# Kernel optimization log

Measured on AMD Instinct MI355X. Metric: run time of the kernel, lower is better.

## Reference

```python
import jax, jax.numpy as jnp
import numpy as np

N_NODES = 50000
N_REL = 4
N_EDGES = 400000
IN_F, HID_F, OUT_F = 128, 128, 64


def _graphconv(h, s, d, W, b, n_nodes):
    """DGL GraphConv, norm='both': D_dst^{-1/2} A D_src^{-1/2} h W + b.
    Degrees clamped to min 1 (DGL behavior for isolated nodes)."""
    ones = jnp.ones(s.shape[0], h.dtype)
    deg_out = jnp.clip(jax.ops.segment_sum(ones, s, num_segments=n_nodes), 1.0)
    deg_in = jnp.clip(jax.ops.segment_sum(ones, d, num_segments=n_nodes), 1.0)
    # scale src features, transform first (weight applied pre-aggregation)
    hw = (h * jax.lax.rsqrt(deg_out)[:, None]) @ W          # [N, out]
    msg = hw[s]                                              # gather  [E, out]
    agg = jax.ops.segment_sum(msg, d, num_segments=n_nodes)  # scatter [N, out]
    return agg * jax.lax.rsqrt(deg_in)[:, None] + b


def _hetero_layer(h, src, dst, W, b):
    # HeteroGraphConv with aggregate='sum': sum per-relation GraphConv outputs
    n_nodes = h.shape[0]
    out = _graphconv(h, src[0], dst[0], W[0], b[0], n_nodes)
    for r in range(1, W.shape[0]):
        out = out + _graphconv(h, src[r], dst[r], W[r], b[r], n_nodes)
    return out


def setup_inputs() -> dict:
    key = jax.random.key(0)
    k = jax.random.split(key, 6)
    x = jax.random.normal(k[0], (N_NODES, IN_F), dtype=jnp.float32)
    src = jax.random.randint(k[1], (N_REL, N_EDGES), 0, N_NODES, dtype=jnp.int32)
    dst = jax.random.randint(k[2], (N_REL, N_EDGES), 0, N_NODES, dtype=jnp.int32)
    W1 = jax.random.normal(k[3], (N_REL, IN_F, HID_F), dtype=jnp.float32) / np.sqrt(IN_F)
    b1 = jnp.zeros((N_REL, HID_F), dtype=jnp.float32)
    W2 = jax.random.normal(k[4], (N_REL, HID_F, OUT_F), dtype=jnp.float32) / np.sqrt(HID_F)
    b2 = jnp.zeros((N_REL, OUT_F), dtype=jnp.float32)
    return {"x": x, "src": src, "dst": dst, "W1": W1, "b1": b1, "W2": W2, "b2": b2}


def reference(x, src, dst, W1, b1, W2, b2):
    h = _hetero_layer(x, src, dst, W1, b1)
    h = jax.nn.relu(h)
    return _hetero_layer(h, src, dst, W2, b2)
```

## Files before the change

### kernel.cpp

```cpp
#include <hip/hip_runtime.h>
#include <hip/hip_bf16.h>

#define N_NODES 50000
#define N_REL 4
#define N_EDGES 400000
#define CHUNK 1024
#define NCHUNK ((N_NODES + CHUNK - 1) / CHUNK)

#define EB 32
#define ECH (N_EDGES / EB)
#define NR 8
#define RNG (N_NODES / NR)

using short8 = __attribute__((ext_vector_type(8))) short;
using f32x4 = __attribute__((ext_vector_type(4))) float;

static __device__ inline unsigned short f2bf(float f) {
  unsigned u = __float_as_uint(f);
  unsigned r = (u + 0x7FFFu + ((u >> 16) & 1u)) >> 16;
  return (unsigned short)r;
}
static __device__ inline float bf2f(unsigned short b) {
  return __uint_as_float(((unsigned)b) << 16);
}
static __device__ inline void fma_bf2(unsigned w, float ds, float& a0,
                                      float& a1) {
  float lo = __uint_as_float(w << 16);
  float hi = __uint_as_float(w & 0xffff0000u);
  a0 = fmaf(lo, ds, a0);
  a1 = fmaf(hi, ds, a1);
}

__global__ __launch_bounds__(256) void k_hist(const int* __restrict__ src,
                                              const int* __restrict__ dst,
                                              unsigned short* __restrict__ Hs,
                                              unsigned short* __restrict__ Hd) {
  const int range = blockIdx.x % NR;
  const int chunk = (blockIdx.x / NR) % EB;
  const int rel = blockIdx.x / (NR * EB);
  __shared__ unsigned int ldsS[RNG / 2], ldsD[RNG / 2];
  for (int i = threadIdx.x; i < RNG / 2; i += 256) {
    ldsS[i] = 0u;
    ldsD[i] = 0u;
  }
  __syncthreads();
  const int n0 = range * RNG;
  const int* sp = src + (size_t)rel * N_EDGES + chunk * ECH;
  const int* dp = dst + (size_t)rel * N_EDGES + chunk * ECH;
  for (int e = threadIdx.x; e < ECH; e += 256) {
    int s = sp[e] - n0;
    if ((unsigned)s < RNG) atomicAdd(&ldsS[s >> 1], 1u << ((s & 1) * 16));
    int d = dp[e] - n0;
    if ((unsigned)d < RNG) atomicAdd(&ldsD[d >> 1], 1u << ((d & 1) * 16));
  }
  __syncthreads();
  unsigned int* HsO =
      (unsigned int*)(Hs + ((size_t)rel * EB + chunk) * N_NODES + n0);
  unsigned int* HdO =
      (unsigned int*)(Hd + ((size_t)rel * EB + chunk) * N_NODES + n0);
  for (int i = threadIdx.x; i < RNG / 2; i += 256) {
    HsO[i] = ldsS[i];
    HdO[i] = ldsD[i];
  }
}

__global__ __launch_bounds__(256) void k_reduce_m(
    const unsigned short* __restrict__ Hs, unsigned short* __restrict__ Hd,
    int* __restrict__ cnt_m, float* __restrict__ dso, float* __restrict__ dsi,
    ushort4* __restrict__ relOff) {
  int n = blockIdx.x * 256 + threadIdx.x;
  if (n >= N_NODES) return;
#pragma unroll
  for (int r = 0; r < N_REL; ++r) {
    int so = 0;
#pragma unroll
    for (int b = 0; b < EB; ++b) so += Hs[((size_t)r * EB + b) * N_NODES + n];
    dso[r * N_NODES + n] = rsqrtf((float)(so < 1 ? 1 : so));
  }
  int run = 0;
  unsigned short rs[4];
#pragma unroll
  for (int r = 0; r < N_REL; ++r) {
    rs[r] = (unsigned short)run;
#pragma unroll
    for (int b = 0; b < EB; ++b) {
      size_t off = ((size_t)r * EB + b) * N_NODES + n;
      int v = Hd[off];
      Hd[off] = (unsigned short)run;
      run += v;
    }
    int di = run - rs[r];
    dsi[r * N_NODES + n] = rsqrtf((float)(di < 1 ? 1 : di));
  }
  cnt_m[n] = run;
  relOff[n] = make_ushort4(rs[0], rs[1], rs[2], rs[3]);
}

__global__ __launch_bounds__(256) void k_chunk_sums(
    const int* __restrict__ cnt_m, int* __restrict__ chunkSums) {
  int c = blockIdx.x;
  int t = threadIdx.x;
  int base = c * CHUNK + t * 4;
  int s = 0;
#pragma unroll
  for (int j = 0; j < 4; ++j) {
    int n = base + j;
    if (n < N_NODES) s += cnt_m[n];
  }
  __shared__ int lds[256];
  lds[t] = s;
  __syncthreads();
  for (int off = 128; off > 0; off >>= 1) {
    if (t < off) lds[t] += lds[t + off];
    __syncthreads();
  }
  if (t == 0) chunkSums[c] = lds[0];
}

__global__ __launch_bounds__(64) void k_scan_chunks(int* __restrict__ chunkSums,
                                                    int* __restrict__ row_ptr) {
  if (threadIdx.x == 0) {
    int running = 0;
    for (int c = 0; c < NCHUNK; ++c) {
      int v = chunkSums[c];
      chunkSums[c] = running;
      running += v;
    }
    row_ptr[N_NODES] = N_REL * N_EDGES;
  }
}

__global__ __launch_bounds__(256) void k_scan_within(
    const int* __restrict__ cnt_m, const int* __restrict__ chunkOff,
    int* __restrict__ row_ptr) {
  int c = blockIdx.x;
  int t = threadIdx.x;
  int base = c * CHUNK + t * 4;
  int v[4];
#pragma unroll
  for (int j = 0; j < 4; ++j) {
    int n = base + j;
    v[j] = (n < N_NODES) ? cnt_m[n] : 0;
  }
  int total = v[0] + v[1] + v[2] + v[3];
  __shared__ int lds[256];
  lds[t] = total;
  __syncthreads();
  for (int off = 1; off < 256; off <<= 1) {
    int add = (t >= off) ? lds[t - off] : 0;
    __syncthreads();
    lds[t] += add;
    __syncthreads();
  }
  int thrExcl = lds[t] - total + chunkOff[c];
  int pre = 0;
#pragma unroll
  for (int j = 0; j < 4; ++j) {
    int n = base + j;
    if (n < N_NODES) row_ptr[n] = thrExcl + pre;
    pre += v[j];
  }
}

__global__ __launch_bounds__(256) void k_fill2m(
    const int* __restrict__ src, const int* __restrict__ dst,
    const unsigned short* __restrict__ Hd, const int* __restrict__ row_ptr,
    int* __restrict__ sorted) {
  const int range = blockIdx.x % NR;
  const int chunk = (blockIdx.x / NR) % EB;
  const int rel = blockIdx.x / (NR * EB);
  __shared__ unsigned int cur[RNG];
  const int n0 = range * RNG;
  const int* rp = row_ptr + n0;
  const unsigned short* pref = Hd + ((size_t)rel * EB + chunk) * N_NODES + n0;
  for (int i = threadIdx.x; i < RNG; i += 256)
    cur[i] = (unsigned)(rp[i] + pref[i]);
  __syncthreads();
  const int* sp = src + (size_t)rel * N_EDGES + chunk * ECH;
  const int* dp = dst + (size_t)rel * N_EDGES + chunk * ECH;
  for (int e = threadIdx.x; e < ECH; e += 256) {
    int d = dp[e] - n0;
    if ((unsigned)d < RNG) {
      unsigned pos = atomicAdd(&cur[d], 1u);
      sorted[pos] = sp[e];
    }
  }
}

__global__ __launch_bounds__(256) void k_prep_x(const float* __restrict__ x,
                                                unsigned short* __restrict__ xb) {
  int i = blockIdx.x * 256 + threadIdx.x;
  if (i >= N_NODES * 16) return;
  const float4* p = (const float4*)x + (size_t)i * 2;
  float4 v0 = p[0], v1 = p[1];
  unsigned short pk[8] = {f2bf(v0.x), f2bf(v0.y), f2bf(v0.z), f2bf(v0.w),
                          f2bf(v1.x), f2bf(v1.y), f2bf(v1.z), f2bf(v1.w)};
  *(uint4*)(xb + (size_t)i * 8) = *(uint4*)pk;
}

__global__ __launch_bounds__(128) void k_prep_w(const float* __restrict__ W1,
                                                const float* __restrict__ W2,
                                                unsigned short* __restrict__ Wt1,
                                                unsigned short* __restrict__ Wt2) {
  int b = blockIdx.x;
  int kk = threadIdx.x;
  if (b < 128) {
    int c = b;
#pragma unroll
    for (int r = 0; r < 4; ++r)
      Wt1[(size_t)c * 512 + r * 128 + kk] =
          f2bf(W1[(size_t)r * 16384 + kk * 128 + c]);
  } else {
    int c = b - 128;
    int r = c >> 6, cc = c & 63;
    Wt2[(size_t)c * 128 + kk] = f2bf(W2[(size_t)r * 8192 + kk * 64 + cc]);
  }
}

__global__ __launch_bounds__(256) void k_gather1a(
    const unsigned short* __restrict__ xb, const int* __restrict__ row_ptr,
    const ushort4* __restrict__ relOff, const int* __restrict__ sortedm,
    const float* __restrict__ dso, const float* __restrict__ dsi,
    unsigned int* __restrict__ agg) {
  const int wave = threadIdx.x >> 6, lane = threadIdx.x & 63;
  const int g = lane & 31;
  const int node = blockIdx.x * 8 + wave * 2 + (lane >> 5);
  const int rp = row_ptr[node], rp1 = row_ptr[node + 1];
  const ushort4 ro = relOff[node];
  const int beg[4] = {rp + ro.x, rp + ro.y, rp + ro.z, rp + ro.w};
  const int end4[4] = {rp + ro.y, rp + ro.z, rp + ro.w, rp1};
#pragma unroll
  for (int r = 0; r < 4; ++r) {
    const float* dsoR = dso + (size_t)r * N_NODES;
    float a0[4] = {0, 0, 0, 0}, a1[4] = {0, 0, 0, 0};
    float a2[4] = {0, 0, 0, 0}, a3[4] = {0, 0, 0, 0};
    for (int base = beg[r]; base < end4[r]; base += 32) {
      int n = end4[r] - base;
      if (n > 32) n = 32;
      int my = (g < n) ? sortedm[base + g] : 0;
      int j = 0;
      for (; j + 3 < n; j += 4) {
#pragma unroll
        for (int k = 0; k < 4; ++k) {
          int s = __shfl(my, j + k, 32);
          float ds = dsoR[s];
          uint2 w = *(const uint2*)(xb + (size_t)s * 128 + g * 4);
          fma_bf2(w.x, ds, a0[k], a1[k]);
          fma_bf2(w.y, ds, a2[k], a3[k]);
        }
      }
      for (; j < n; ++j) {
        int s = __shfl(my, j, 32);
        float ds = dsoR[s];
        uint2 w = *(const uint2*)(xb + (size_t)s * 128 + g * 4);
        fma_bf2(w.x, ds, a0[0], a1[0]);
        fma_bf2(w.y, ds, a2[0], a3[0]);
      }
    }
    float di = dsi[(size_t)r * N_NODES + node];
    float t0 = ((a0[0] + a0[1]) + (a0[2] + a0[3])) * di;
    float t1 = ((a1[0] + a1[1]) + (a1[2] + a1[3])) * di;
    float t2 = ((a2[0] + a2[1]) + (a2[2] + a2[3])) * di;
    float t3 = ((a3[0] + a3[1]) + (a3[2] + a3[3])) * di;
    uint2 pk;
    pk.x = (unsigned)f2bf(t0) | ((unsigned)f2bf(t1) << 16);
    pk.y = (unsigned)f2bf(t2) | ((unsigned)f2bf(t3) << 16);
    *((uint2*)agg + ((size_t)node * 4 + r) * 32 + g) = pk;
  }
}

__global__ __launch_bounds__(256, 2) void k_gemm_h1(
    const unsigned short* __restrict__ agg, const unsigned short* __restrict__ Wt,
    const float* __restrict__ b1, unsigned short* __restrict__ h1, int M) {
  __shared__ unsigned short Alds[64 * 128];
  __shared__ unsigned short Wlds[128 * 128];
  const int tid = threadIdx.x;
  const int wid = tid >> 6, lane = tid & 63;
  const int rowBase = blockIdx.x * 64;
  const int lrow = lane & 15;
  const int quarter = lane >> 4;

  f32x4 acc[4][2];
#pragma unroll
  for (int i = 0; i < 4; ++i)
#pragma unroll
    for (int j = 0; j < 2; ++j) acc[i][j] = (f32x4){0.f, 0.f, 0.f, 0.f};

  for (int k0 = 0; k0 < 4; ++k0) {
    __syncthreads();
#pragma unroll
    for (int it = 0; it < 4; ++it) {
      int cid = tid + it * 256;
      int row = cid >> 4, kg = cid & 15;
      int grow = rowBase + row;
      uint4 v = make_uint4(0, 0, 0, 0);
      if (grow < M)
        v = *(const uint4*)(agg + (size_t)grow * 512 + k0 * 128 + kg * 8);
      *(uint4*)(Alds + row * 128 + ((kg ^ (row & 7)) * 8)) = v;
    }
#pragma unroll
    for (int it = 0; it < 8; ++it) {
      int cid = tid + it * 256;
      int c = cid >> 4, kg = cid & 15;
      uint4 v = *(const uint4*)(Wt + (size_t)c * 512 + k0 * 128 + kg * 8);
      *(uint4*)(Wlds + c * 128 + ((kg ^ (c & 7)) * 8)) = v;
    }
    __syncthreads();
#pragma unroll
    for (int kk = 0; kk < 4; ++kk) {
      int kg = kk * 4 + quarter;
      short8 a[4], b[2];
#pragma unroll
      for (int i = 0; i < 4; ++i) {
        int row = i * 16 + lrow;
        a[i] = *(const short8*)(Alds + row * 128 + ((kg ^ (row & 7)) * 8));
      }
#pragma unroll
      for (int j = 0; j < 2; ++j) {
        int c = wid * 32 + j * 16 + lrow;
        b[j] = *(const short8*)(Wlds + c * 128 + ((kg ^ (c & 7)) * 8));
      }
#pragma unroll
      for (int i = 0; i < 4; ++i)
#pragma unroll
        for (int j = 0; j < 2; ++j)
          acc[i][j] = __builtin_amdgcn_mfma_f32_16x16x32_bf16(a[i], b[j],
                                                              acc[i][j], 0, 0, 0);
    }
  }

#pragma unroll
  for (int j = 0; j < 2; ++j) {
    int c = wid * 32 + j * 16 + lrow;
    float bs = b1[c] + b1[128 + c] + b1[256 + c] + b1[384 + c];
#pragma unroll
    for (int i = 0; i < 4; ++i) {
#pragma unroll
      for (int r = 0; r < 4; ++r) {
        int grow = rowBase + i * 16 + quarter * 4 + r;
        if (grow < M)
          h1[(size_t)grow * 128 + c] = f2bf(fmaxf(acc[i][j][r] + bs, 0.f));
      }
    }
  }
}

template <int REL_COLS>
__global__ __launch_bounds__(256, 2) void k_gemm_mfma(
    const unsigned short* __restrict__ A, const unsigned short* __restrict__ Wt,
    const float* __restrict__ dsoBase, unsigned short* __restrict__ C,
    int cstride, int M) {
  __shared__ unsigned short Alds[64 * 128];
  __shared__ unsigned short Wlds[256 * 128];
  const int tid = threadIdx.x;
  const int wid = tid >> 6, lane = tid & 63;
  const int rowBase = blockIdx.x * 64;

#pragma unroll
  for (int i = 0; i < 4; ++i) {
    int cid = tid + i * 256;
    int row = cid >> 4, kg = cid & 15;
    int grow = rowBase + row;
    uint4 v = make_uint4(0, 0, 0, 0);
    if (grow < M) v = *(const uint4*)(A + (size_t)grow * 128 + kg * 8);
    *(uint4*)(Alds + row * 128 + ((kg ^ (row & 7)) * 8)) = v;
  }
#pragma unroll
  for (int i = 0; i < 16; ++i) {
    int cid = tid + i * 256;
    int row = cid >> 4, kg = cid & 15;
    uint4 v = *(const uint4*)(Wt + (size_t)row * 128 + kg * 8);
    *(uint4*)(Wlds + row * 128 + ((kg ^ (row & 7)) * 8)) = v;
  }
  __syncthreads();

  f32x4 acc[4][4];
#pragma unroll
  for (int i = 0; i < 4; ++i)
#pragma unroll
    for (int j = 0; j < 4; ++j) acc[i][j] = (f32x4){0.f, 0.f, 0.f, 0.f};

  const int lrow = lane & 15;
  const int khalf = lane >> 4;
#pragma unroll
  for (int k0 = 0; k0 < 4; ++k0) {
    int kg = k0 * 4 + khalf;
    short8 a[4], b[4];
#pragma unroll
    for (int i = 0; i < 4; ++i) {
      int row = i * 16 + lrow;
      a[i] = *(const short8*)(Alds + row * 128 + ((kg ^ (row & 7)) * 8));
    }
#pragma unroll
    for (int j = 0; j < 4; ++j) {
      int wrow = wid * 64 + j * 16 + lrow;
      b[j] = *(const short8*)(Wlds + wrow * 128 + ((kg ^ (wrow & 7)) * 8));
    }
#pragma unroll
    for (int i = 0; i < 4; ++i)
#pragma unroll
      for (int j = 0; j < 4; ++j)
        acc[i][j] = __builtin_amdgcn_mfma_f32_16x16x32_bf16(a[i], b[j],
                                                            acc[i][j], 0, 0, 0);
  }

#pragma unroll
  for (int i = 0; i < 4; ++i) {
#pragma unroll
    for (int j = 0; j < 4; ++j) {
      int col = wid * 64 + j * 16 + (lane & 15);
      const float* dsoCol = dsoBase + (size_t)(col / REL_COLS) * N_NODES;
#pragma unroll
      for (int r = 0; r < 4; ++r) {
        int grow = rowBase + i * 16 + (lane >> 4) * 4 + r;
        if (grow < M)
          C[(size_t)grow * cstride + col] = f2bf(acc[i][j][r] * dsoCol[grow]);
      }
    }
  }
}

__global__ __launch_bounds__(256) void k_gather2m(
    const unsigned short* __restrict__ Y, const int* __restrict__ row_ptr,
    const ushort4* __restrict__ relOff, const int* __restrict__ sortedm,
    const float* __restrict__ dsi, const float* __restrict__ b2,
    float* __restrict__ out) {
  const int wave = threadIdx.x >> 6, lane = threadIdx.x & 63;
  const int g = lane & 15;
  const int node = blockIdx.x * 16 + wave * 4 + (lane >> 4);
  const int rp = row_ptr[node], rp1 = row_ptr[node + 1];
  const ushort4 ro = relOff[node];
  const int beg[4] = {rp + ro.x, rp + ro.y, rp + ro.z, rp + ro.w};
  const int end4[4] = {rp + ro.y, rp + ro.z, rp + ro.w, rp1};
  float t0 = 0.f, t1 = 0.f, t2 = 0.f, t3 = 0.f;
#pragma unroll
  for (int r = 0; r < 4; ++r) {
    float a0[4] = {0, 0, 0, 0}, a1[4] = {0, 0, 0, 0};
    float a2[4] = {0, 0, 0, 0}, a3[4] = {0, 0, 0, 0};
    for (int base = beg[r]; base < end4[r]; base += 16) {
      int n = end4[r] - base;
      if (n > 16) n = 16;
      int my = (g < n) ? sortedm[base + g] : 0;
      int j = 0;
      for (; j + 3 < n; j += 4) {
#pragma unroll
        for (int k = 0; k < 4; ++k) {
          int s = __shfl(my, j + k, 16);
          uint2 w = *(const uint2*)(Y + ((size_t)s * 4 + r) * 64 + g * 4);
          fma_bf2(w.x, 1.f, a0[k], a1[k]);
          fma_bf2(w.y, 1.f, a2[k], a3[k]);
        }
      }
      for (; j < n; ++j) {
        int s = __shfl(my, j, 16);
        uint2 w = *(const uint2*)(Y + ((size_t)s * 4 + r) * 64 + g * 4);
        fma_bf2(w.x, 1.f, a0[0], a1[0]);
        fma_bf2(w.y, 1.f, a2[0], a3[0]);
      }
    }
    float di = dsi[(size_t)r * N_NODES + node];
    t0 = fmaf((a0[0] + a0[1]) + (a0[2] + a0[3]), di, t0);
    t1 = fmaf((a1[0] + a1[1]) + (a1[2] + a1[3]), di, t1);
    t2 = fmaf((a2[0] + a2[1]) + (a2[2] + a2[3]), di, t2);
    t3 = fmaf((a3[0] + a3[1]) + (a3[2] + a3[3]), di, t3);
  }
#pragma unroll
  for (int r = 0; r < 4; ++r) {
    float4 bb = *(const float4*)(b2 + r * 64 + g * 4);
    t0 += bb.x;
    t1 += bb.y;
    t2 += bb.z;
    t3 += bb.w;
  }
  *(float4*)(out + (size_t)node * 64 + g * 4) = make_float4(t0, t1, t2, t3);
}

extern "C" void kernel_launch(void* const* d_in, const int* in_sizes, int n_in,
                              void* d_out, int out_size, void* d_ws,
                              size_t ws_size, hipStream_t stream) {
  const float* x  = (const float*)d_in[0];
  const int* src  = (const int*)d_in[1];
  const int* dst  = (const int*)d_in[2];
  const float* W1 = (const float*)d_in[3];
  const float* b1 = (const float*)d_in[4];
  const float* W2 = (const float*)d_in[5];
  const float* b2 = (const float*)d_in[6];
  float* out = (float*)d_out;

  char* wsb = (char*)d_ws;
  unsigned short* Hs = (unsigned short*)wsb;
  unsigned short* h1 = (unsigned short*)wsb;
  unsigned short* Hd = Hs + (size_t)N_REL * EB * N_NODES;
  unsigned short* xb = Hd + (size_t)N_REL * EB * N_NODES;
  unsigned short* agg = xb + (size_t)N_NODES * 128;
  unsigned short* Y2 = agg;
  char* tail = (char*)(agg + (size_t)N_NODES * 512);
  unsigned short* Wt1 = (unsigned short*)tail;
  unsigned short* Wt2 = Wt1 + 128 * 512;
  float* dso = (float*)(Wt2 + 256 * 128);
  float* dsi = dso + N_REL * N_NODES;
  ushort4* relOff = (ushort4*)(dsi + N_REL * N_NODES);
  int* cnt_m = (int*)(relOff + N_NODES);
  int* row_ptr = cnt_m + N_NODES;
  int* chunkSums = row_ptr + (N_NODES + 1);
  int* sorted = chunkSums + 64;

  k_prep_x<<<(N_NODES * 16 + 255) / 256, 256, 0, stream>>>(x, xb);
  k_prep_w<<<384, 128, 0, stream>>>(W1, W2, Wt1, Wt2);
  k_hist<<<N_REL * EB * NR, 256, 0, stream>>>(src, dst, Hs, Hd);
  k_reduce_m<<<(N_NODES + 255) / 256, 256, 0, stream>>>(Hs, Hd, cnt_m, dso,
                                                        dsi, relOff);
  k_chunk_sums<<<NCHUNK, 256, 0, stream>>>(cnt_m, chunkSums);
  k_scan_chunks<<<1, 64, 0, stream>>>(chunkSums, row_ptr);
  k_scan_within<<<NCHUNK, 256, 0, stream>>>(cnt_m, chunkSums, row_ptr);
  k_fill2m<<<N_REL * EB * NR, 256, 0, stream>>>(src, dst, Hd, row_ptr, sorted);

  k_gather1a<<<N_NODES / 8, 256, 0, stream>>>(xb, row_ptr, relOff, sorted, dso,
                                              dsi, (unsigned int*)agg);
  k_gemm_h1<<<(N_NODES + 63) / 64, 256, 0, stream>>>(agg, Wt1, b1, h1,
                                                     N_NODES);
  k_gemm_mfma<64><<<(N_NODES + 63) / 64, 256, 0, stream>>>(h1, Wt2, dso, Y2,
                                                           256, N_NODES);
  k_gather2m<<<N_NODES / 16, 256, 0, stream>>>(Y2, row_ptr, relOff, sorted,
                                               dsi, b2, out);
}
```

Baseline: 275.2 us.

## Fuse prep and histogram kernels, fold chunk sums into reduce, flatten gather loops

Merges the x conversion, weight transpose and degree histogram kernels into one launch, and folds the per-chunk edge-count sum into the degree-reduce kernel through block reductions plus atomics. This removes two kernel launches and their serialization gaps. Both gather kernels now walk a node's whole edge list in a single windowed loop that switches relation at boundaries. This replaces separate per-relation loops that each reloaded index windows and underfilled the shuffle windows. The price is heavier per-block divergence in the fused kernel and extra branching inside the gather loops.

```diff
diff --git a/kernel.cpp b/kernel.cpp
--- a/kernel.cpp
+++ b/kernel.cpp
@@ -11,6 +11,10 @@
 #define ECH (N_EDGES / EB)
 #define NR 8
 #define RNG (N_NODES / NR)
+
+#define PX_BLOCKS 3125
+#define PW_BLOCKS 192
+#define HIST_BLOCKS (N_REL * EB * NR)
 
 using short8 = __attribute__((ext_vector_type(8))) short;
 using f32x4 = __attribute__((ext_vector_type(4))) float;
@@ -31,15 +35,47 @@
   a1 = fmaf(hi, ds, a1);
 }
 
-__global__ __launch_bounds__(256) void k_hist(const int* __restrict__ src,
-                                              const int* __restrict__ dst,
-                                              unsigned short* __restrict__ Hs,
-                                              unsigned short* __restrict__ Hd) {
-  const int range = blockIdx.x % NR;
-  const int chunk = (blockIdx.x / NR) % EB;
-  const int rel = blockIdx.x / (NR * EB);
+__global__ __launch_bounds__(256) void k_prep_fused(
+    const float* __restrict__ x, const float* __restrict__ W1,
+    const float* __restrict__ W2, const int* __restrict__ src,
+    const int* __restrict__ dst, unsigned short* __restrict__ xb,
+    unsigned short* __restrict__ Wt1, unsigned short* __restrict__ Wt2,
+    unsigned short* __restrict__ Hs, unsigned short* __restrict__ Hd,
+    int* __restrict__ chunkSums) {
   __shared__ unsigned int ldsS[RNG / 2], ldsD[RNG / 2];
-  for (int i = threadIdx.x; i < RNG / 2; i += 256) {
+  const int b = blockIdx.x;
+  const int tid = threadIdx.x;
+  if (b < PX_BLOCKS) {
+    if (b == 0 && tid < 64) chunkSums[tid] = 0;
+    int i = b * 256 + tid;
+    const float4* p = (const float4*)x + (size_t)i * 2;
+    float4 v0 = p[0], v1 = p[1];
+    unsigned short pk[8] = {f2bf(v0.x), f2bf(v0.y), f2bf(v0.z), f2bf(v0.w),
+                            f2bf(v1.x), f2bf(v1.y), f2bf(v1.z), f2bf(v1.w)};
+    *(uint4*)(xb + (size_t)i * 8) = *(uint4*)pk;
+    return;
+  }
+  if (b < PX_BLOCKS + PW_BLOCKS) {
+    int ob = (b - PX_BLOCKS) * 2 + (tid >> 7);
+    int kk = tid & 127;
+    if (ob < 128) {
+      int c = ob;
+#pragma unroll
+      for (int r = 0; r < 4; ++r)
+        Wt1[(size_t)c * 512 + r * 128 + kk] =
+            f2bf(W1[(size_t)r * 16384 + kk * 128 + c]);
+    } else {
+      int c = ob - 128;
+      int r = c >> 6, cc = c & 63;
+      Wt2[(size_t)c * 128 + kk] = f2bf(W2[(size_t)r * 8192 + kk * 64 + cc]);
+    }
+    return;
+  }
+  const int hb = b - PX_BLOCKS - PW_BLOCKS;
+  const int range = hb % NR;
+  const int chunk = (hb / NR) % EB;
+  const int rel = hb / (NR * EB);
+  for (int i = tid; i < RNG / 2; i += 256) {
     ldsS[i] = 0u;
     ldsD[i] = 0u;
   }
@@ -47,7 +83,7 @@
   const int n0 = range * RNG;
   const int* sp = src + (size_t)rel * N_EDGES + chunk * ECH;
   const int* dp = dst + (size_t)rel * N_EDGES + chunk * ECH;
-  for (int e = threadIdx.x; e < ECH; e += 256) {
+  for (int e = tid; e < ECH; e += 256) {
     int s = sp[e] - n0;
     if ((unsigned)s < RNG) atomicAdd(&ldsS[s >> 1], 1u << ((s & 1) * 16));
     int d = dp[e] - n0;
@@ -58,7 +94,7 @@
       (unsigned int*)(Hs + ((size_t)rel * EB + chunk) * N_NODES + n0);
   unsigned int* HdO =
       (unsigned int*)(Hd + ((size_t)rel * EB + chunk) * N_NODES + n0);
-  for (int i = threadIdx.x; i < RNG / 2; i += 256) {
+  for (int i = tid; i < RNG / 2; i += 256) {
     HsO[i] = ldsS[i];
     HdO[i] = ldsD[i];
   }
@@ -67,54 +103,43 @@
 __global__ __launch_bounds__(256) void k_reduce_m(
     const unsigned short* __restrict__ Hs, unsigned short* __restrict__ Hd,
     int* __restrict__ cnt_m, float* __restrict__ dso, float* __restrict__ dsi,
-    ushort4* __restrict__ relOff) {
+    ushort4* __restrict__ relOff, int* __restrict__ chunkSums) {
   int n = blockIdx.x * 256 + threadIdx.x;
-  if (n >= N_NODES) return;
-#pragma unroll
-  for (int r = 0; r < N_REL; ++r) {
-    int so = 0;
-#pragma unroll
-    for (int b = 0; b < EB; ++b) so += Hs[((size_t)r * EB + b) * N_NODES + n];
-    dso[r * N_NODES + n] = rsqrtf((float)(so < 1 ? 1 : so));
-  }
   int run = 0;
-  unsigned short rs[4];
-#pragma unroll
-  for (int r = 0; r < N_REL; ++r) {
-    rs[r] = (unsigned short)run;
-#pragma unroll
-    for (int b = 0; b < EB; ++b) {
-      size_t off = ((size_t)r * EB + b) * N_NODES + n;
-      int v = Hd[off];
-      Hd[off] = (unsigned short)run;
-      run += v;
-    }
-    int di = run - rs[r];
-    dsi[r * N_NODES + n] = rsqrtf((float)(di < 1 ? 1 : di));
-  }
-  cnt_m[n] = run;
-  relOff[n] = make_ushort4(rs[0], rs[1], rs[2], rs[3]);
-}
-
-__global__ __launch_bounds__(256) void k_chunk_sums(
-    const int* __restrict__ cnt_m, int* __restrict__ chunkSums) {
-  int c = blockIdx.x;
-  int t = threadIdx.x;
-  int base = c * CHUNK + t * 4;
-  int s = 0;
-#pragma unroll
-  for (int j = 0; j < 4; ++j) {
-    int n = base + j;
-    if (n < N_NODES) s += cnt_m[n];
-  }
-  __shared__ int lds[256];
-  lds[t] = s;
+  if (n < N_NODES) {
+#pragma unroll
+    for (int r = 0; r < N_REL; ++r) {
+      int so = 0;
+#pragma unroll
+      for (int b = 0; b < EB; ++b)
+        so += Hs[((size_t)r * EB + b) * N_NODES + n];
+      dso[r * N_NODES + n] = rsqrtf((float)(so < 1 ? 1 : so));
+    }
+    unsigned short rs[4];
+#pragma unroll
+    for (int r = 0; r < N_REL; ++r) {
+      rs[r] = (unsigned short)run;
+#pragma unroll
+      for (int b = 0; b < EB; ++b) {
+        size_t off = ((size_t)r * EB + b) * N_NODES + n;
+        int v = Hd[off];
+        Hd[off] = (unsigned short)run;
+        run += v;
+      }
+      int di = run - rs[r];
+      dsi[r * N_NODES + n] = rsqrtf((float)(di < 1 ? 1 : di));
+    }
+    cnt_m[n] = run;
+    relOff[n] = make_ushort4(rs[0], rs[1], rs[2], rs[3]);
+  }
+  __shared__ int red[256];
+  red[threadIdx.x] = run;
   __syncthreads();
   for (int off = 128; off > 0; off >>= 1) {
-    if (t < off) lds[t] += lds[t + off];
+    if (threadIdx.x < off) red[threadIdx.x] += red[threadIdx.x + off];
     __syncthreads();
   }
-  if (t == 0) chunkSums[c] = lds[0];
+  if (threadIdx.x == 0) atomicAdd(&chunkSums[blockIdx.x >> 2], red[0]);
 }
 
 __global__ __launch_bounds__(64) void k_scan_chunks(int* __restrict__ chunkSums,
@@ -187,36 +212,6 @@
   }
 }
 
-__global__ __launch_bounds__(256) void k_prep_x(const float* __restrict__ x,
-                                                unsigned short* __restrict__ xb) {
-  int i = blockIdx.x * 256 + threadIdx.x;
-  if (i >= N_NODES * 16) return;
-  const float4* p = (const float4*)x + (size_t)i * 2;
-  float4 v0 = p[0], v1 = p[1];
-  unsigned short pk[8] = {f2bf(v0.x), f2bf(v0.y), f2bf(v0.z), f2bf(v0.w),
-                          f2bf(v1.x), f2bf(v1.y), f2bf(v1.z), f2bf(v1.w)};
-  *(uint4*)(xb + (size_t)i * 8) = *(uint4*)pk;
-}
-
-__global__ __launch_bounds__(128) void k_prep_w(const float* __restrict__ W1,
-                                                const float* __restrict__ W2,
-                                                unsigned short* __restrict__ Wt1,
-                                                unsigned short* __restrict__ Wt2) {
-  int b = blockIdx.x;
-  int kk = threadIdx.x;
-  if (b < 128) {
-    int c = b;
-#pragma unroll
-    for (int r = 0; r < 4; ++r)
-      Wt1[(size_t)c * 512 + r * 128 + kk] =
-          f2bf(W1[(size_t)r * 16384 + kk * 128 + c]);
-  } else {
-    int c = b - 128;
-    int r = c >> 6, cc = c & 63;
-    Wt2[(size_t)c * 128 + kk] = f2bf(W2[(size_t)r * 8192 + kk * 64 + cc]);
-  }
-}
-
 __global__ __launch_bounds__(256) void k_gather1a(
     const unsigned short* __restrict__ xb, const int* __restrict__ row_ptr,
     const ushort4* __restrict__ relOff, const int* __restrict__ sortedm,
@@ -225,47 +220,90 @@
   const int wave = threadIdx.x >> 6, lane = threadIdx.x & 63;
   const int g = lane & 31;
   const int node = blockIdx.x * 8 + wave * 2 + (lane >> 5);
-  const int rp = row_ptr[node], rp1 = row_ptr[node + 1];
-  const ushort4 ro = relOff[node];
-  const int beg[4] = {rp + ro.x, rp + ro.y, rp + ro.z, rp + ro.w};
-  const int end4[4] = {rp + ro.y, rp + ro.z, rp + ro.w, rp1};
-#pragma unroll
-  for (int r = 0; r < 4; ++r) {
-    const float* dsoR = dso + (size_t)r * N_NODES;
-    float a0[4] = {0, 0, 0, 0}, a1[4] = {0, 0, 0, 0};
-    float a2[4] = {0, 0, 0, 0}, a3[4] = {0, 0, 0, 0};
-    for (int base = beg[r]; base < end4[r]; base += 32) {
-      int n = end4[r] - base;
-      if (n > 32) n = 32;
-      int my = (g < n) ? sortedm[base + g] : 0;
-      int j = 0;
-      for (; j + 3 < n; j += 4) {
+  const int rp = row_ptr[node];
+  const int nt = row_ptr[node + 1] - rp;
+  const ushort4 ro4 = relOff[node];
+  const int rb1 = ro4.y, rb2 = ro4.z, rb3 = ro4.w;
+
+  float rs[4][4];
+#pragma unroll
+  for (int r = 0; r < 4; ++r)
+#pragma unroll
+    for (int f = 0; f < 4; ++f) rs[r][f] = 0.f;
+  float acc[4][4];
+#pragma unroll
+  for (int f = 0; f < 4; ++f)
+#pragma unroll
+    for (int k = 0; k < 4; ++k) acc[f][k] = 0.f;
+
+#define FLUSH1(RR)                                                     \
+  {                                                                    \
+    rs[RR][0] += (acc[0][0] + acc[0][1]) + (acc[0][2] + acc[0][3]);    \
+    rs[RR][1] += (acc[1][0] + acc[1][1]) + (acc[1][2] + acc[1][3]);    \
+    rs[RR][2] += (acc[2][0] + acc[2][1]) + (acc[2][2] + acc[2][3]);    \
+    rs[RR][3] += (acc[3][0] + acc[3][1]) + (acc[3][2] + acc[3][3]);    \
+    _Pragma("unroll") for (int f = 0; f < 4; ++f)                      \
+        _Pragma("unroll") for (int k = 0; k < 4; ++k) acc[f][k] = 0.f; \
+  }
+
+  int r = 0;
+  int rend = rb1;
+  for (int w0 = 0; w0 < nt; w0 += 32) {
+    int wn = nt - w0;
+    if (wn > 32) wn = 32;
+    int my = (g < wn) ? sortedm[rp + w0 + g] : 0;
+    int j = 0;
+    while (j < wn) {
+      while (w0 + j >= rend) {
+        switch (r) {
+          case 0: FLUSH1(0); break;
+          case 1: FLUSH1(1); break;
+          default: FLUSH1(2); break;
+        }
+        ++r;
+        rend = (r == 1) ? rb2 : (r == 2) ? rb3 : nt;
+      }
+      int lim = rend - w0;
+      if (lim > wn) lim = wn;
+      const float* dsoR = dso + (size_t)r * N_NODES;
+      for (; j + 3 < lim; j += 4) {
 #pragma unroll
         for (int k = 0; k < 4; ++k) {
           int s = __shfl(my, j + k, 32);
           float ds = dsoR[s];
           uint2 w = *(const uint2*)(xb + (size_t)s * 128 + g * 4);
-          fma_bf2(w.x, ds, a0[k], a1[k]);
-          fma_bf2(w.y, ds, a2[k], a3[k]);
+          fma_bf2(w.x, ds, acc[0][k], acc[1][k]);
+          fma_bf2(w.y, ds, acc[2][k], acc[3][k]);
         }
       }
-      for (; j < n; ++j) {
+      for (; j < lim; ++j) {
         int s = __shfl(my, j, 32);
         float ds = dsoR[s];
         uint2 w = *(const uint2*)(xb + (size_t)s * 128 + g * 4);
-        fma_bf2(w.x, ds, a0[0], a1[0]);
-        fma_bf2(w.y, ds, a2[0], a3[0]);
-      }
-    }
-    float di = dsi[(size_t)r * N_NODES + node];
-    float t0 = ((a0[0] + a0[1]) + (a0[2] + a0[3])) * di;
-    float t1 = ((a1[0] + a1[1]) + (a1[2] + a1[3])) * di;
-    float t2 = ((a2[0] + a2[1]) + (a2[2] + a2[3])) * di;
-    float t3 = ((a3[0] + a3[1]) + (a3[2] + a3[3])) * di;
+        fma_bf2(w.x, ds, acc[0][0], acc[1][0]);
+        fma_bf2(w.y, ds, acc[2][0], acc[3][0]);
+      }
+    }
+  }
+  switch (r) {
+    case 0: FLUSH1(0); break;
+    case 1: FLUSH1(1); break;
+    case 2: FLUSH1(2); break;
+    default: FLUSH1(3); break;
+  }
+#undef FLUSH1
+
+  float dia[4] = {dsi[node], dsi[N_NODES + node], dsi[2 * N_NODES + node],
+                  dsi[3 * N_NODES + node]};
+#pragma unroll
+  for (int rr = 0; rr < 4; ++rr) {
+    float di = dia[rr];
     uint2 pk;
-    pk.x = (unsigned)f2bf(t0) | ((unsigned)f2bf(t1) << 16);
-    pk.y = (unsigned)f2bf(t2) | ((unsigned)f2bf(t3) << 16);
-    *((uint2*)agg + ((size_t)node * 4 + r) * 32 + g) = pk;
+    pk.x = (unsigned)f2bf(rs[rr][0] * di) |
+           ((unsigned)f2bf(rs[rr][1] * di) << 16);
+    pk.y = (unsigned)f2bf(rs[rr][2] * di) |
+           ((unsigned)f2bf(rs[rr][3] * di) << 16);
+    *((uint2*)agg + ((size_t)node * 4 + rr) * 32 + g) = pk;
   }
 }
 
@@ -428,51 +466,85 @@
   const int wave = threadIdx.x >> 6, lane = threadIdx.x & 63;
   const int g = lane & 15;
   const int node = blockIdx.x * 16 + wave * 4 + (lane >> 4);
-  const int rp = row_ptr[node], rp1 = row_ptr[node + 1];
-  const ushort4 ro = relOff[node];
-  const int beg[4] = {rp + ro.x, rp + ro.y, rp + ro.z, rp + ro.w};
-  const int end4[4] = {rp + ro.y, rp + ro.z, rp + ro.w, rp1};
-  float t0 = 0.f, t1 = 0.f, t2 = 0.f, t3 = 0.f;
-#pragma unroll
-  for (int r = 0; r < 4; ++r) {
-    float a0[4] = {0, 0, 0, 0}, a1[4] = {0, 0, 0, 0};
-    float a2[4] = {0, 0, 0, 0}, a3[4] = {0, 0, 0, 0};
-    for (int base = beg[r]; base < end4[r]; base += 16) {
-      int n = end4[r] - base;
-      if (n > 16) n = 16;
-      int my = (g < n) ? sortedm[base + g] : 0;
-      int j = 0;
-      for (; j + 3 < n; j += 4) {
+  const int rp = row_ptr[node];
+  const int nt = row_ptr[node + 1] - rp;
+  const ushort4 ro4 = relOff[node];
+  const int rb1 = ro4.y, rb2 = ro4.z, rb3 = ro4.w;
+  const float dia[4] = {dsi[node], dsi[N_NODES + node],
+                        dsi[2 * N_NODES + node], dsi[3 * N_NODES + node]};
+
+  float t[4] = {0.f, 0.f, 0.f, 0.f};
+  float acc[4][4];
+#pragma unroll
+  for (int f = 0; f < 4; ++f)
+#pragma unroll
+    for (int k = 0; k < 4; ++k) acc[f][k] = 0.f;
+
+#define FLUSH2(RR)                                                          \
+  {                                                                         \
+    float di = dia[RR];                                                     \
+    t[0] = fmaf((acc[0][0] + acc[0][1]) + (acc[0][2] + acc[0][3]), di, t[0]); \
+    t[1] = fmaf((acc[1][0] + acc[1][1]) + (acc[1][2] + acc[1][3]), di, t[1]); \
+    t[2] = fmaf((acc[2][0] + acc[2][1]) + (acc[2][2] + acc[2][3]), di, t[2]); \
+    t[3] = fmaf((acc[3][0] + acc[3][1]) + (acc[3][2] + acc[3][3]), di, t[3]); \
+    _Pragma("unroll") for (int f = 0; f < 4; ++f)                           \
+        _Pragma("unroll") for (int k = 0; k < 4; ++k) acc[f][k] = 0.f;      \
+  }
+
+  int r = 0;
+  int rend = rb1;
+  for (int w0 = 0; w0 < nt; w0 += 16) {
+    int wn = nt - w0;
+    if (wn > 16) wn = 16;
+    int my = (g < wn) ? sortedm[rp + w0 + g] : 0;
+    int j = 0;
+    while (j < wn) {
+      while (w0 + j >= rend) {
+        switch (r) {
+          case 0: FLUSH2(0); break;
+          case 1: FLUSH2(1); break;
+          default: FLUSH2(2); break;
+        }
+        ++r;
+        rend = (r == 1) ? rb2 : (r == 2) ? rb3 : nt;
+      }
+      int lim = rend - w0;
+      if (lim > wn) lim = wn;
+      for (; j + 3 < lim; j += 4) {
 #pragma unroll
         for (int k = 0; k < 4; ++k) {
           int s = __shfl(my, j + k, 16);
           uint2 w = *(const uint2*)(Y + ((size_t)s * 4 + r) * 64 + g * 4);
-          fma_bf2(w.x, 1.f, a0[k], a1[k]);
-          fma_bf2(w.y, 1.f, a2[k], a3[k]);
+          fma_bf2(w.x, 1.f, acc[0][k], acc[1][k]);
+          fma_bf2(w.y, 1.f, acc[2][k], acc[3][k]);
         }
       }
-      for (; j < n; ++j) {
+      for (; j < lim; ++j) {
         int s = __shfl(my, j, 16);
         uint2 w = *(const uint2*)(Y + ((size_t)s * 4 + r) * 64 + g * 4);
-        fma_bf2(w.x, 1.f, a0[0], a1[0]);
-        fma_bf2(w.y, 1.f, a2[0], a3[0]);
-      }
-    }
-    float di = dsi[(size_t)r * N_NODES + node];
-    t0 = fmaf((a0[0] + a0[1]) + (a0[2] + a0[3]), di, t0);
-    t1 = fmaf((a1[0] + a1[1]) + (a1[2] + a1[3]), di, t1);
-    t2 = fmaf((a2[0] + a2[1]) + (a2[2] + a2[3]), di, t2);
-    t3 = fmaf((a3[0] + a3[1]) + (a3[2] + a3[3]), di, t3);
-  }
-#pragma unroll
-  for (int r = 0; r < 4; ++r) {
-    float4 bb = *(const float4*)(b2 + r * 64 + g * 4);
-    t0 += bb.x;
-    t1 += bb.y;
-    t2 += bb.z;
-    t3 += bb.w;
-  }
-  *(float4*)(out + (size_t)node * 64 + g * 4) = make_float4(t0, t1, t2, t3);
+        fma_bf2(w.x, 1.f, acc[0][0], acc[1][0]);
+        fma_bf2(w.y, 1.f, acc[2][0], acc[3][0]);
+      }
+    }
+  }
+  switch (r) {
+    case 0: FLUSH2(0); break;
+    case 1: FLUSH2(1); break;
+    case 2: FLUSH2(2); break;
+    default: FLUSH2(3); break;
+  }
+#undef FLUSH2
+
+#pragma unroll
+  for (int rr = 0; rr < 4; ++rr) {
+    float4 bb = *(const float4*)(b2 + rr * 64 + g * 4);
+    t[0] += bb.x;
+    t[1] += bb.y;
+    t[2] += bb.z;
+    t[3] += bb.w;
+  }
+  *(float4*)(out + (size_t)node * 64 + g * 4) =
+      make_float4(t[0], t[1], t[2], t[3]);
 }
 
 extern "C" void kernel_launch(void* const* d_in, const int* in_sizes, int n_in,
@@ -505,12 +577,10 @@
   int* chunkSums = row_ptr + (N_NODES + 1);
   int* sorted = chunkSums + 64;
 
-  k_prep_x<<<(N_NODES * 16 + 255) / 256, 256, 0, stream>>>(x, xb);
-  k_prep_w<<<384, 128, 0, stream>>>(W1, W2, Wt1, Wt2);
-  k_hist<<<N_REL * EB * NR, 256, 0, stream>>>(src, dst, Hs, Hd);
+  k_prep_fused<<<PX_BLOCKS + PW_BLOCKS + HIST_BLOCKS, 256, 0, stream>>>(
+      x, W1, W2, src, dst, xb, Wt1, Wt2, Hs, Hd, chunkSums);
   k_reduce_m<<<(N_NODES + 255) / 256, 256, 0, stream>>>(Hs, Hd, cnt_m, dso,
-                                                        dsi, relOff);
-  k_chunk_sums<<<NCHUNK, 256, 0, stream>>>(cnt_m, chunkSums);
+                                                        dsi, relOff, chunkSums);
   k_scan_chunks<<<1, 64, 0, stream>>>(chunkSums, row_ptr);
   k_scan_within<<<NCHUNK, 256, 0, stream>>>(cnt_m, chunkSums, row_ptr);
   k_fill2m<<<N_REL * EB * NR, 256, 0, stream>>>(src, dst, Hd, row_ptr, sorted);
```

Result: faster. 267.2 us (-2.9%).

## Fuse prep kernels, fold chunk sums into reduce, split gather1 by feature quarter

Applied to the files above, without the earlier changes.

Merges the x/W bf16 conversion and the degree histogram into one kernel, and folds the per-chunk sum into k_reduce_m using atomics. Together these remove two launches. The layer-1 gather is restructured so that 8 lanes per node each handle a 32-feature quarter, with four block groups covering the quarters. This raises node-level parallelism and shrinks the per-batch edge window, but it rereads the edge lists and degree scales once per quarter.

```diff
diff --git a/kernel.cpp b/kernel.cpp
--- a/kernel.cpp
+++ b/kernel.cpp
@@ -11,6 +11,12 @@
 #define ECH (N_EDGES / EB)
 #define NR 8
 #define RNG (N_NODES / NR)
+
+#define PX_BLOCKS 3125
+#define PW_BLOCKS 192
+#define HIST_BLOCKS (N_REL * EB * NR)
+
+#define G1_BLOCKS 1563
 
 using short8 = __attribute__((ext_vector_type(8))) short;
 using f32x4 = __attribute__((ext_vector_type(4))) float;
@@ -31,15 +37,47 @@
   a1 = fmaf(hi, ds, a1);
 }
 
-__global__ __launch_bounds__(256) void k_hist(const int* __restrict__ src,
-                                              const int* __restrict__ dst,
-                                              unsigned short* __restrict__ Hs,
-                                              unsigned short* __restrict__ Hd) {
-  const int range = blockIdx.x % NR;
-  const int chunk = (blockIdx.x / NR) % EB;
-  const int rel = blockIdx.x / (NR * EB);
+__global__ __launch_bounds__(256) void k_prep_fused(
+    const float* __restrict__ x, const float* __restrict__ W1,
+    const float* __restrict__ W2, const int* __restrict__ src,
+    const int* __restrict__ dst, unsigned short* __restrict__ xb,
+    unsigned short* __restrict__ Wt1, unsigned short* __restrict__ Wt2,
+    unsigned short* __restrict__ Hs, unsigned short* __restrict__ Hd,
+    int* __restrict__ chunkSums) {
   __shared__ unsigned int ldsS[RNG / 2], ldsD[RNG / 2];
-  for (int i = threadIdx.x; i < RNG / 2; i += 256) {
+  const int b = blockIdx.x;
+  const int tid = threadIdx.x;
+  if (b < PX_BLOCKS) {
+    if (b == 0 && tid < 64) chunkSums[tid] = 0;
+    int i = b * 256 + tid;
+    const float4* p = (const float4*)x + (size_t)i * 2;
+    float4 v0 = p[0], v1 = p[1];
+    unsigned short pk[8] = {f2bf(v0.x), f2bf(v0.y), f2bf(v0.z), f2bf(v0.w),
+                            f2bf(v1.x), f2bf(v1.y), f2bf(v1.z), f2bf(v1.w)};
+    *(uint4*)(xb + (size_t)i * 8) = *(uint4*)pk;
+    return;
+  }
+  if (b < PX_BLOCKS + PW_BLOCKS) {
+    int ob = (b - PX_BLOCKS) * 2 + (tid >> 7);
+    int kk = tid & 127;
+    if (ob < 128) {
+      int c = ob;
+#pragma unroll
+      for (int r = 0; r < 4; ++r)
+        Wt1[(size_t)c * 512 + r * 128 + kk] =
+            f2bf(W1[(size_t)r * 16384 + kk * 128 + c]);
+    } else {
+      int c = ob - 128;
+      int r = c >> 6, cc = c & 63;
+      Wt2[(size_t)c * 128 + kk] = f2bf(W2[(size_t)r * 8192 + kk * 64 + cc]);
+    }
+    return;
+  }
+  const int hb = b - PX_BLOCKS - PW_BLOCKS;
+  const int range = hb % NR;
+  const int chunk = (hb / NR) % EB;
+  const int rel = hb / (NR * EB);
+  for (int i = tid; i < RNG / 2; i += 256) {
     ldsS[i] = 0u;
     ldsD[i] = 0u;
   }
@@ -47,7 +85,7 @@
   const int n0 = range * RNG;
   const int* sp = src + (size_t)rel * N_EDGES + chunk * ECH;
   const int* dp = dst + (size_t)rel * N_EDGES + chunk * ECH;
-  for (int e = threadIdx.x; e < ECH; e += 256) {
+  for (int e = tid; e < ECH; e += 256) {
     int s = sp[e] - n0;
     if ((unsigned)s < RNG) atomicAdd(&ldsS[s >> 1], 1u << ((s & 1) * 16));
     int d = dp[e] - n0;
@@ -58,7 +96,7 @@
       (unsigned int*)(Hs + ((size_t)rel * EB + chunk) * N_NODES + n0);
   unsigned int* HdO =
       (unsigned int*)(Hd + ((size_t)rel * EB + chunk) * N_NODES + n0);
-  for (int i = threadIdx.x; i < RNG / 2; i += 256) {
+  for (int i = tid; i < RNG / 2; i += 256) {
     HsO[i] = ldsS[i];
     HdO[i] = ldsD[i];
   }
@@ -67,54 +105,43 @@
 __global__ __launch_bounds__(256) void k_reduce_m(
     const unsigned short* __restrict__ Hs, unsigned short* __restrict__ Hd,
     int* __restrict__ cnt_m, float* __restrict__ dso, float* __restrict__ dsi,
-    ushort4* __restrict__ relOff) {
+    ushort4* __restrict__ relOff, int* __restrict__ chunkSums) {
   int n = blockIdx.x * 256 + threadIdx.x;
-  if (n >= N_NODES) return;
-#pragma unroll
-  for (int r = 0; r < N_REL; ++r) {
-    int so = 0;
-#pragma unroll
-    for (int b = 0; b < EB; ++b) so += Hs[((size_t)r * EB + b) * N_NODES + n];
-    dso[r * N_NODES + n] = rsqrtf((float)(so < 1 ? 1 : so));
-  }
   int run = 0;
-  unsigned short rs[4];
-#pragma unroll
-  for (int r = 0; r < N_REL; ++r) {
-    rs[r] = (unsigned short)run;
-#pragma unroll
-    for (int b = 0; b < EB; ++b) {
-      size_t off = ((size_t)r * EB + b) * N_NODES + n;
-      int v = Hd[off];
-      Hd[off] = (unsigned short)run;
-      run += v;
-    }
-    int di = run - rs[r];
-    dsi[r * N_NODES + n] = rsqrtf((float)(di < 1 ? 1 : di));
-  }
-  cnt_m[n] = run;
-  relOff[n] = make_ushort4(rs[0], rs[1], rs[2], rs[3]);
-}
-
-__global__ __launch_bounds__(256) void k_chunk_sums(
-    const int* __restrict__ cnt_m, int* __restrict__ chunkSums) {
-  int c = blockIdx.x;
-  int t = threadIdx.x;
-  int base = c * CHUNK + t * 4;
-  int s = 0;
-#pragma unroll
-  for (int j = 0; j < 4; ++j) {
-    int n = base + j;
-    if (n < N_NODES) s += cnt_m[n];
-  }
-  __shared__ int lds[256];
-  lds[t] = s;
+  if (n < N_NODES) {
+#pragma unroll
+    for (int r = 0; r < N_REL; ++r) {
+      int so = 0;
+#pragma unroll
+      for (int b = 0; b < EB; ++b)
+        so += Hs[((size_t)r * EB + b) * N_NODES + n];
+      dso[r * N_NODES + n] = rsqrtf((float)(so < 1 ? 1 : so));
+    }
+    unsigned short rs[4];
+#pragma unroll
+    for (int r = 0; r < N_REL; ++r) {
+      rs[r] = (unsigned short)run;
+#pragma unroll
+      for (int b = 0; b < EB; ++b) {
+        size_t off = ((size_t)r * EB + b) * N_NODES + n;
+        int v = Hd[off];
+        Hd[off] = (unsigned short)run;
+        run += v;
+      }
+      int di = run - rs[r];
+      dsi[r * N_NODES + n] = rsqrtf((float)(di < 1 ? 1 : di));
+    }
+    cnt_m[n] = run;
+    relOff[n] = make_ushort4(rs[0], rs[1], rs[2], rs[3]);
+  }
+  __shared__ int red[256];
+  red[threadIdx.x] = run;
   __syncthreads();
   for (int off = 128; off > 0; off >>= 1) {
-    if (t < off) lds[t] += lds[t + off];
+    if (threadIdx.x < off) red[threadIdx.x] += red[threadIdx.x + off];
     __syncthreads();
   }
-  if (t == 0) chunkSums[c] = lds[0];
+  if (threadIdx.x == 0) atomicAdd(&chunkSums[blockIdx.x >> 2], red[0]);
 }
 
 __global__ __launch_bounds__(64) void k_scan_chunks(int* __restrict__ chunkSums,
@@ -187,72 +214,46 @@
   }
 }
 
-__global__ __launch_bounds__(256) void k_prep_x(const float* __restrict__ x,
-                                                unsigned short* __restrict__ xb) {
-  int i = blockIdx.x * 256 + threadIdx.x;
-  if (i >= N_NODES * 16) return;
-  const float4* p = (const float4*)x + (size_t)i * 2;
-  float4 v0 = p[0], v1 = p[1];
-  unsigned short pk[8] = {f2bf(v0.x), f2bf(v0.y), f2bf(v0.z), f2bf(v0.w),
-                          f2bf(v1.x), f2bf(v1.y), f2bf(v1.z), f2bf(v1.w)};
-  *(uint4*)(xb + (size_t)i * 8) = *(uint4*)pk;
-}
-
-__global__ __launch_bounds__(128) void k_prep_w(const float* __restrict__ W1,
-                                                const float* __restrict__ W2,
-                                                unsigned short* __restrict__ Wt1,
-                                                unsigned short* __restrict__ Wt2) {
-  int b = blockIdx.x;
-  int kk = threadIdx.x;
-  if (b < 128) {
-    int c = b;
-#pragma unroll
-    for (int r = 0; r < 4; ++r)
-      Wt1[(size_t)c * 512 + r * 128 + kk] =
-          f2bf(W1[(size_t)r * 16384 + kk * 128 + c]);
-  } else {
-    int c = b - 128;
-    int r = c >> 6, cc = c & 63;
-    Wt2[(size_t)c * 128 + kk] = f2bf(W2[(size_t)r * 8192 + kk * 64 + cc]);
-  }
-}
-
 __global__ __launch_bounds__(256) void k_gather1a(
     const unsigned short* __restrict__ xb, const int* __restrict__ row_ptr,
     const ushort4* __restrict__ relOff, const int* __restrict__ sortedm,
     const float* __restrict__ dso, const float* __restrict__ dsi,
     unsigned int* __restrict__ agg) {
+  const int fq = blockIdx.x / G1_BLOCKS;
+  const int nb = blockIdx.x % G1_BLOCKS;
   const int wave = threadIdx.x >> 6, lane = threadIdx.x & 63;
-  const int g = lane & 31;
-  const int node = blockIdx.x * 8 + wave * 2 + (lane >> 5);
+  const int g = lane & 7;
+  const int node = nb * 32 + wave * 8 + (lane >> 3);
+  if (node >= N_NODES) return;
   const int rp = row_ptr[node], rp1 = row_ptr[node + 1];
   const ushort4 ro = relOff[node];
   const int beg[4] = {rp + ro.x, rp + ro.y, rp + ro.z, rp + ro.w};
   const int end4[4] = {rp + ro.y, rp + ro.z, rp + ro.w, rp1};
+  const unsigned short* xq = xb + fq * 32 + g * 4;
 #pragma unroll
   for (int r = 0; r < 4; ++r) {
     const float* dsoR = dso + (size_t)r * N_NODES;
     float a0[4] = {0, 0, 0, 0}, a1[4] = {0, 0, 0, 0};
     float a2[4] = {0, 0, 0, 0}, a3[4] = {0, 0, 0, 0};
-    for (int base = beg[r]; base < end4[r]; base += 32) {
+    for (int base = beg[r]; base < end4[r]; base += 8) {
       int n = end4[r] - base;
-      if (n > 32) n = 32;
+      if (n > 8) n = 8;
       int my = (g < n) ? sortedm[base + g] : 0;
       int j = 0;
       for (; j + 3 < n; j += 4) {
 #pragma unroll
         for (int k = 0; k < 4; ++k) {
-          int s = __shfl(my, j + k, 32);
+          int s = __shfl(my, j + k, 8);
           float ds = dsoR[s];
-          uint2 w = *(const uint2*)(xb + (size_t)s * 128 + g * 4);
+          uint2 w = *(const uint2*)(xq + (size_t)s * 128);
           fma_bf2(w.x, ds, a0[k], a1[k]);
           fma_bf2(w.y, ds, a2[k], a3[k]);
         }
       }
       for (; j < n; ++j) {
-        int s = __shfl(my, j, 32);
+        int s = __shfl(my, j, 8);
         float ds = dsoR[s];
-        uint2 w = *(const uint2*)(xb + (size_t)s * 128 + g * 4);
+        uint2 w = *(const uint2*)(xq + (size_t)s * 128);
         fma_bf2(w.x, ds, a0[0], a1[0]);
         fma_bf2(w.y, ds, a2[0], a3[0]);
       }
@@ -265,7 +266,7 @@
     uint2 pk;
     pk.x = (unsigned)f2bf(t0) | ((unsigned)f2bf(t1) << 16);
     pk.y = (unsigned)f2bf(t2) | ((unsigned)f2bf(t3) << 16);
-    *((uint2*)agg + ((size_t)node * 4 + r) * 32 + g) = pk;
+    *((uint2*)agg + ((size_t)node * 4 + r) * 32 + fq * 8 + g) = pk;
   }
 }
 
@@ -505,18 +506,16 @@
   int* chunkSums = row_ptr + (N_NODES + 1);
   int* sorted = chunkSums + 64;
 
-  k_prep_x<<<(N_NODES * 16 + 255) / 256, 256, 0, stream>>>(x, xb);
-  k_prep_w<<<384, 128, 0, stream>>>(W1, W2, Wt1, Wt2);
-  k_hist<<<N_REL * EB * NR, 256, 0, stream>>>(src, dst, Hs, Hd);
+  k_prep_fused<<<PX_BLOCKS + PW_BLOCKS + HIST_BLOCKS, 256, 0, stream>>>(
+      x, W1, W2, src, dst, xb, Wt1, Wt2, Hs, Hd, chunkSums);
   k_reduce_m<<<(N_NODES + 255) / 256, 256, 0, stream>>>(Hs, Hd, cnt_m, dso,
-                                                        dsi, relOff);
-  k_chunk_sums<<<NCHUNK, 256, 0, stream>>>(cnt_m, chunkSums);
+                                                        dsi, relOff, chunkSums);
   k_scan_chunks<<<1, 64, 0, stream>>>(chunkSums, row_ptr);
   k_scan_within<<<NCHUNK, 256, 0, stream>>>(cnt_m, chunkSums, row_ptr);
   k_fill2m<<<N_REL * EB * NR, 256, 0, stream>>>(src, dst, Hd, row_ptr, sorted);
 
-  k_gather1a<<<N_NODES / 8, 256, 0, stream>>>(xb, row_ptr, relOff, sorted, dso,
-                                              dsi, (unsigned int*)agg);
+  k_gather1a<<<4 * G1_BLOCKS, 256, 0, stream>>>(xb, row_ptr, relOff, sorted,
+                                                dso, dsi, (unsigned int*)agg);
   k_gemm_h1<<<(N_NODES + 63) / 64, 256, 0, stream>>>(agg, Wt1, b1, h1,
                                                      N_NODES);
   k_gemm_mfma<64><<<(N_NODES + 63) / 64, 256, 0, stream>>>(h1, Wt2, dso, Y2,
```

New measurement: 320.7 us. +16.5%, slower.
